# Optimization experiments

Hardware: AMD Instinct MI355X
Metric: run time of the kernel (lower is better)

## Reference

```python
import jax, jax.numpy as jnp
import numpy as np

N_NODES = 100000
N_EDGES = 1600000
IN_C, HID_C, OUT_C = 256, 128, 40
NEG_SLOPE = 0.2


def _gat_conv(x, W, att_l, att_r, b, src, dst, n_nodes):
    # x: [N, in], W: [out, in] (torch Linear layout)
    xl = x @ W.T                                  # [N, C]
    alpha_l = (xl * att_l).sum(-1)                # [N]
    alpha_r = (xl * att_r).sum(-1)                # [N]
    e = alpha_l[src] + alpha_r[dst]               # [E]
    e = jax.nn.leaky_relu(e, NEG_SLOPE)
    # segment softmax over destination nodes
    seg_max = jax.ops.segment_max(e, dst, num_segments=n_nodes)
    seg_max = jnp.where(jnp.isfinite(seg_max), seg_max, 0.0)
    ex = jnp.exp(e - seg_max[dst])
    denom = jax.ops.segment_sum(ex, dst, num_segments=n_nodes)
    alpha = ex / jnp.maximum(denom, 1e-16)[dst]   # [E]
    msgs = xl[src] * alpha[:, None]               # [E, C]
    out = jax.ops.segment_sum(msgs, dst, num_segments=n_nodes)
    return out + b


def setup_inputs() -> dict:
    key = jax.random.key(0)
    ks = jax.random.split(key, 9)
    def glorot(k, shape, fan):
        return jax.random.normal(k, shape, jnp.float32) * (1.0 / np.sqrt(fan))
    x = jax.random.normal(ks[0], (N_NODES, IN_C), jnp.float32)
    edge_index = jax.random.randint(ks[1], (2, N_EDGES), 0, N_NODES, jnp.int32)
    return {
        "x": x,
        "edge_index": edge_index,
        "W1": glorot(ks[2], (HID_C, IN_C), IN_C),
        "att_l1": glorot(ks[3], (HID_C,), HID_C),
        "att_r1": glorot(ks[4], (HID_C,), HID_C),
        "b1": jnp.zeros((HID_C,), jnp.float32),
        "W2": glorot(ks[5], (OUT_C, HID_C), HID_C),
        "att_l2": glorot(ks[6], (OUT_C,), OUT_C),
        "att_r2": glorot(ks[7], (OUT_C,), OUT_C),
        "b2": jnp.zeros((OUT_C,), jnp.float32),
    }


def reference(x, edge_index, W1, att_l1, att_r1, b1, W2, att_l2, att_r2, b2):
    src, dst = edge_index[0], edge_index[1]
    n = x.shape[0]
    # eval mode: dropout is identity
    h = _gat_conv(x, W1, att_l1, att_r1, b1, src, dst, n)
    h = jax.nn.elu(h)
    h = _gat_conv(h, W2, att_l2, att_r2, b2, src, dst, n)
    return jax.nn.log_softmax(h, axis=1)
```

## Files before the change

kernel.cpp:

```cpp
#include <hip/hip_runtime.h>
#include <hip/hip_bf16.h>

#define N_NODES 100000
#define N_EDGES 1600000
#define IN_C 256
#define HID_C 128
#define OUT_C 40
#define NB1 391

typedef short bf16x8 __attribute__((ext_vector_type(8)));
typedef float f32x4 __attribute__((ext_vector_type(4)));

__device__ __forceinline__ float lrelu(float x) { return x > 0.f ? x : 0.2f * x; }
__device__ __forceinline__ float eluf(float x) { return x > 0.f ? x : expm1f(x); }
__device__ __forceinline__ unsigned short f2bf(float f) {
    unsigned u = __float_as_uint(f);
    unsigned r = (u + 0x7FFFu + ((u >> 16) & 1u)) >> 16;
    return (unsigned short)r;
}

__global__ __launch_bounds__(256) void zero_cnt_kernel(unsigned* __restrict__ cnt)
{
    int i = blockIdx.x * 256 + threadIdx.x;
    if (i < N_NODES) cnt[i] = 0u;
}

__global__ __launch_bounds__(256) void rank_kernel(const int* __restrict__ dst,
                                                   unsigned* __restrict__ cnt,
                                                   unsigned* __restrict__ rank)
{
    int e4 = (blockIdx.x * 256 + threadIdx.x) * 4;
    if (e4 >= N_EDGES) return;
    int4 d = *(const int4*)(dst + e4);
    uint4 r;
    r.x = atomicAdd(&cnt[d.x], 1u);
    r.y = atomicAdd(&cnt[d.y], 1u);
    r.z = atomicAdd(&cnt[d.z], 1u);
    r.w = atomicAdd(&cnt[d.w], 1u);
    *(uint4*)(rank + e4) = r;
}

__global__ __launch_bounds__(256) void scan1_kernel(const unsigned* __restrict__ cnt,
                                                    unsigned* __restrict__ partial,
                                                    unsigned* __restrict__ blocksum)
{
    int gid = blockIdx.x * 256 + threadIdx.x;
    unsigned v = (gid < N_NODES) ? cnt[gid] : 0u;
    unsigned orig = v;
    int lane = threadIdx.x & 63, w = threadIdx.x >> 6;
#pragma unroll
    for (int o = 1; o < 64; o <<= 1) {
        unsigned t = __shfl_up(v, o);
        if (lane >= o) v += t;
    }
    __shared__ unsigned wsum[4];
    if (lane == 63) wsum[w] = v;
    __syncthreads();
    unsigned off = 0;
    for (int i = 0; i < w; ++i) off += wsum[i];
    v += off;
    if (gid < N_NODES) partial[gid] = v - orig;
    if (threadIdx.x == 255) blocksum[blockIdx.x] = v;
}

__global__ __launch_bounds__(512) void scan2_kernel(unsigned* __restrict__ blocksum)
{
    int tid = threadIdx.x;
    unsigned v = (tid < NB1) ? blocksum[tid] : 0u;
    unsigned orig = v;
    int lane = tid & 63, w = tid >> 6;
#pragma unroll
    for (int o = 1; o < 64; o <<= 1) {
        unsigned t = __shfl_up(v, o);
        if (lane >= o) v += t;
    }
    __shared__ unsigned wsum[8];
    if (lane == 63) wsum[w] = v;
    __syncthreads();
    unsigned off = 0;
    for (int i = 0; i < w; ++i) off += wsum[i];
    v += off;
    if (tid < NB1) blocksum[tid] = v - orig;
}

__global__ __launch_bounds__(256) void scan3_kernel(const unsigned* __restrict__ partial,
                                                    const unsigned* __restrict__ blocksum,
                                                    unsigned* __restrict__ row_start)
{
    int gid = blockIdx.x * 256 + threadIdx.x;
    if (gid < N_NODES) row_start[gid] = partial[gid] + blocksum[gid >> 8];
}

__global__ __launch_bounds__(256) void place_kernel(const int* __restrict__ src,
                                                    const int* __restrict__ dst,
                                                    const unsigned* __restrict__ rank,
                                                    const unsigned* __restrict__ row_start,
                                                    int* __restrict__ csr_src)
{
    int e4 = (blockIdx.x * 256 + threadIdx.x) * 4;
    if (e4 >= N_EDGES) return;
    int4 d = *(const int4*)(dst + e4);
    int4 s = *(const int4*)(src + e4);
    uint4 r = *(const uint4*)(rank + e4);
    csr_src[row_start[d.x] + r.x] = s.x;
    csr_src[row_start[d.y] + r.y] = s.y;
    csr_src[row_start[d.z] + r.z] = s.z;
    csr_src[row_start[d.w] + r.w] = s.w;
}

template <int KD, int PC>
__global__ __launch_bounds__(256) void prep_w_kernel(const float* __restrict__ W,
                                                     unsigned short* __restrict__ Wb,
                                                     int realC)
{
    int idx = blockIdx.x * 256 + threadIdx.x;
    if (idx >= PC * KD) return;
    int ch = idx / KD;
    int k = idx & (KD - 1);
    float v = (ch < realC) ? W[(size_t)ch * KD + k] : 0.f;
    Wb[idx] = f2bf(v);
}

template <int KD, int NT, int COLS>
__global__ __launch_bounds__(256) void gemm_mfma_kernel(
    const float* __restrict__ A, const unsigned short* __restrict__ Wb,
    float* __restrict__ out)
{
    int tid = threadIdx.x;
    int wv = tid >> 6, lane = tid & 63;
    int bm = blockIdx.x * 64 + wv * 16;
    int r = lane & 15;
    int kg = lane >> 4;

    f32x4 acc[NT];
#pragma unroll
    for (int n = 0; n < NT; ++n) acc[n] = (f32x4){0.f, 0.f, 0.f, 0.f};

    int arow = bm + r; if (arow >= N_NODES) arow = N_NODES - 1;
    const float* ap = A + (size_t)arow * KD + kg * 8;
    const unsigned short* bp = Wb + (size_t)r * KD + kg * 8;

    for (int ks = 0; ks < KD / 32; ++ks) {
        float4 a0 = *(const float4*)(ap);
        float4 a1 = *(const float4*)(ap + 4);
        bf16x8 af;
        af[0] = (short)f2bf(a0.x); af[1] = (short)f2bf(a0.y);
        af[2] = (short)f2bf(a0.z); af[3] = (short)f2bf(a0.w);
        af[4] = (short)f2bf(a1.x); af[5] = (short)f2bf(a1.y);
        af[6] = (short)f2bf(a1.z); af[7] = (short)f2bf(a1.w);
#pragma unroll
        for (int n = 0; n < NT; ++n) {
            bf16x8 bf_ = *(const bf16x8*)(bp + (size_t)n * 16 * KD);
            acc[n] = __builtin_amdgcn_mfma_f32_16x16x32_bf16(af, bf_, acc[n], 0, 0, 0);
        }
        ap += 32; bp += 32;
    }

#pragma unroll
    for (int n = 0; n < NT; ++n) {
        int col = n * 16 + r;
        if (col < COLS) {
#pragma unroll
            for (int rr = 0; rr < 4; ++rr) {
                int node = bm + kg * 4 + rr;
                if (node < N_NODES) out[(size_t)node * COLS + col] = acc[n][rr];
            }
        }
    }
}

template <int C>
__global__ __launch_bounds__(256) void alphas_kernel(
    const float* __restrict__ xl, const float* __restrict__ attl,
    const float* __restrict__ attr, float* __restrict__ al, float* __restrict__ ar)
{
    int wid = blockIdx.x * 4 + (threadIdx.x >> 6);
    int lane = threadIdx.x & 63;
    if (wid >= N_NODES) return;
    const float* row = xl + (size_t)wid * C;
    float sl = 0.f, sr = 0.f;
    if (lane < C) { float v = row[lane]; sl += v * attl[lane]; sr += v * attr[lane]; }
    if (C > 64 && lane + 64 < C) { float v = row[lane + 64]; sl += v * attl[lane + 64]; sr += v * attr[lane + 64]; }
#pragma unroll
    for (int o = 32; o > 0; o >>= 1) { sl += __shfl_xor(sl, o); sr += __shfl_xor(sr, o); }
    if (lane == 0) { al[wid] = sl; ar[wid] = sr; }
}

template <int C, int MODE>
__global__ __launch_bounds__(256) void agg_kernel(
    const int* __restrict__ csr_src,
    const unsigned* __restrict__ row_start, const unsigned* __restrict__ deg,
    const float* __restrict__ al, const float* __restrict__ ar,
    const float* __restrict__ xl, const float* __restrict__ bias,
    float* __restrict__ outp)
{
    int node = blockIdx.x * 4 + (threadIdx.x >> 6);
    int lane = threadIdx.x & 63;
    if (node >= N_NODES) return;
    unsigned beg = row_start[node];
    unsigned end = beg + deg[node];
    float ar_d = ar[node];

    unsigned i0 = beg + lane;
    float e0 = (i0 < end) ? lrelu(al[csr_src[i0]] + ar_d) : -INFINITY;
    float m_l = e0;
    for (unsigned i = i0 + 64; i < end; i += 64)
        m_l = fmaxf(m_l, lrelu(al[csr_src[i]] + ar_d));
    float mx = m_l;
#pragma unroll
    for (int o = 32; o > 0; o >>= 1) mx = fmaxf(mx, __shfl_xor(mx, o));
    float s_l = (i0 < end) ? __expf(e0 - mx) : 0.f;
    for (unsigned i = i0 + 64; i < end; i += 64)
        s_l += __expf(lrelu(al[csr_src[i]] + ar_d) - mx);
    float sm = s_l;
#pragma unroll
    for (int o = 32; o > 0; o >>= 1) sm += __shfl_xor(sm, o);
    float inv = 1.f / fmaxf(sm, 1e-16f);

    float acc0 = 0.f, acc1 = 0.f;
    unsigned i = beg;
    for (; i + 4 <= end; i += 4) {
        int s0 = csr_src[i], s1 = csr_src[i + 1], s2 = csr_src[i + 2], s3 = csr_src[i + 3];
        float w0 = __expf(lrelu(al[s0] + ar_d) - mx);
        float w1 = __expf(lrelu(al[s1] + ar_d) - mx);
        float w2 = __expf(lrelu(al[s2] + ar_d) - mx);
        float w3 = __expf(lrelu(al[s3] + ar_d) - mx);
        const float* p0 = xl + (size_t)s0 * C;
        const float* p1 = xl + (size_t)s1 * C;
        const float* p2 = xl + (size_t)s2 * C;
        const float* p3 = xl + (size_t)s3 * C;
        if (C > 64) {
            acc0 += p0[lane] * w0;      acc1 += p0[lane + 64] * w0;
            acc0 += p1[lane] * w1;      acc1 += p1[lane + 64] * w1;
            acc0 += p2[lane] * w2;      acc1 += p2[lane + 64] * w2;
            acc0 += p3[lane] * w3;      acc1 += p3[lane + 64] * w3;
        } else if (lane < C) {
            acc0 += p0[lane] * w0 + p1[lane] * w1 + p2[lane] * w2 + p3[lane] * w3;
        }
    }
    for (; i < end; ++i) {
        int s0 = csr_src[i];
        float w0 = __expf(lrelu(al[s0] + ar_d) - mx);
        const float* p0 = xl + (size_t)s0 * C;
        if (C > 64) { acc0 += p0[lane] * w0; acc1 += p0[lane + 64] * w0; }
        else if (lane < C) acc0 += p0[lane] * w0;
    }
    acc0 *= inv; acc1 *= inv;

    if (MODE == 0) {
        outp[(size_t)node * C + lane]      = eluf(acc0 + bias[lane]);
        outp[(size_t)node * C + lane + 64] = eluf(acc1 + bias[lane + 64]);
    } else {
        float v = (lane < C) ? (acc0 + bias[lane]) : -INFINITY;
        float m = v;
#pragma unroll
        for (int o = 32; o > 0; o >>= 1) m = fmaxf(m, __shfl_xor(m, o));
        float ex = (lane < C) ? __expf(v - m) : 0.f;
        float ssum = ex;
#pragma unroll
        for (int o = 32; o > 0; o >>= 1) ssum += __shfl_xor(ssum, o);
        if (lane < C) outp[(size_t)node * C + lane] = v - m - logf(ssum);
    }
}

extern "C" void kernel_launch(void* const* d_in, const int* in_sizes, int n_in,
                              void* d_out, int out_size, void* d_ws, size_t ws_size,
                              hipStream_t stream)
{
    const float* x    = (const float*)d_in[0];
    const int*   ei   = (const int*)d_in[1];
    const float* W1   = (const float*)d_in[2];
    const float* atl1 = (const float*)d_in[3];
    const float* atr1 = (const float*)d_in[4];
    const float* b1   = (const float*)d_in[5];
    const float* W2   = (const float*)d_in[6];
    const float* atl2 = (const float*)d_in[7];
    const float* atr2 = (const float*)d_in[8];
    const float* b2   = (const float*)d_in[9];
    float* out = (float*)d_out;
    const int* src = ei;
    const int* dst = ei + N_EDGES;
    (void)ws_size; (void)n_in; (void)in_sizes; (void)out_size;

    float* ws = (float*)d_ws;
    float* xl1      = ws;
    float* h        = xl1 + (size_t)N_NODES * HID_C;
    float* xl2      = h   + (size_t)N_NODES * HID_C;
    float* al1      = xl2 + (size_t)N_NODES * OUT_C;
    float* ar1      = al1 + N_NODES;
    float* al2      = ar1 + N_NODES;
    float* ar2      = al2 + N_NODES;
    unsigned* cnt      = (unsigned*)(ar2 + N_NODES);
    unsigned* partial  = cnt + N_NODES;
    unsigned* blocksum = partial + N_NODES;
    unsigned* row_start= blocksum + 512;
    int*      csr_src  = (int*)(row_start + N_NODES);
    unsigned short* W1b = (unsigned short*)(csr_src + N_EDGES);
    unsigned short* W2b = W1b + HID_C * IN_C;
    unsigned* rank = (unsigned*)xl2;

    const int EB4 = (N_EDGES / 4 + 255) / 256;
    const int NB4 = (N_NODES + 3) / 4;

    zero_cnt_kernel<<<NB1, 256, 0, stream>>>(cnt);
    rank_kernel<<<EB4, 256, 0, stream>>>(dst, cnt, rank);
    scan1_kernel<<<NB1, 256, 0, stream>>>(cnt, partial, blocksum);
    scan2_kernel<<<1, 512, 0, stream>>>(blocksum);
    scan3_kernel<<<NB1, 256, 0, stream>>>(partial, blocksum, row_start);
    place_kernel<<<EB4, 256, 0, stream>>>(src, dst, rank, row_start, csr_src);

    prep_w_kernel<IN_C, HID_C><<<(HID_C * IN_C + 255) / 256, 256, 0, stream>>>(W1, W1b, HID_C);
    prep_w_kernel<HID_C, 48><<<(48 * HID_C + 255) / 256, 256, 0, stream>>>(W2, W2b, OUT_C);

    gemm_mfma_kernel<IN_C, 8, HID_C><<<(N_NODES + 63) / 64, 256, 0, stream>>>(x, W1b, xl1);
    alphas_kernel<HID_C><<<NB4, 256, 0, stream>>>(xl1, atl1, atr1, al1, ar1);
    agg_kernel<HID_C, 0><<<NB4, 256, 0, stream>>>(
        csr_src, row_start, cnt, al1, ar1, xl1, b1, h);

    gemm_mfma_kernel<HID_C, 3, OUT_C><<<(N_NODES + 63) / 64, 256, 0, stream>>>(h, W2b, xl2);
    alphas_kernel<OUT_C><<<NB4, 256, 0, stream>>>(xl2, atl2, atr2, al2, ar2);
    agg_kernel<OUT_C, 1><<<NB4, 256, 0, stream>>>(
        csr_src, row_start, cnt, al2, ar2, xl2, b2, out);
}
```

Baseline: 599.4 us.

## Store intermediate node features in bf16 to halve gather traffic

The projected features xl1, the hidden activations h and xl2 are now stored as bf16 instead of fp32. The aggregation and alpha kernels read packed bf16 pairs per lane. The second GEMM consumes bf16 directly, which removes the in-loop conversion. The goal is to cut memory bandwidth in the edge-gather aggregation, the dominant cost, at the price of lower precision in the intermediates.

```diff
diff --git a/kernel.cpp b/kernel.cpp
--- a/kernel.cpp
+++ b/kernel.cpp
@@ -18,6 +18,8 @@
     unsigned r = (u + 0x7FFFu + ((u >> 16) & 1u)) >> 16;
     return (unsigned short)r;
 }
+__device__ __forceinline__ float bf_lo(unsigned u) { return __uint_as_float(u << 16); }
+__device__ __forceinline__ float bf_hi(unsigned u) { return __uint_as_float(u & 0xFFFF0000u); }
 
 __global__ __launch_bounds__(256) void zero_cnt_kernel(unsigned* __restrict__ cnt)
 {
@@ -121,11 +123,11 @@
     Wb[idx] = f2bf(v);
 }
 
-template <int KD, int NT, int COLS>
-__global__ __launch_bounds__(256) void gemm_mfma_kernel(
+__global__ __launch_bounds__(256) void gemm1_mfma_kernel(
     const float* __restrict__ A, const unsigned short* __restrict__ Wb,
-    float* __restrict__ out)
-{
+    unsigned short* __restrict__ outb)
+{
+    const int KD = IN_C, NT = 8, COLS = HID_C;
     int tid = threadIdx.x;
     int wv = tid >> 6, lane = tid & 63;
     int bm = blockIdx.x * 64 + wv * 16;
@@ -159,11 +161,51 @@
 #pragma unroll
     for (int n = 0; n < NT; ++n) {
         int col = n * 16 + r;
+#pragma unroll
+        for (int rr = 0; rr < 4; ++rr) {
+            int node = bm + kg * 4 + rr;
+            if (node < N_NODES) outb[(size_t)node * COLS + col] = f2bf(acc[n][rr]);
+        }
+    }
+}
+
+__global__ __launch_bounds__(256) void gemm2_mfma_kernel(
+    const unsigned short* __restrict__ Ab, const unsigned short* __restrict__ Wb,
+    unsigned short* __restrict__ outb)
+{
+    const int KD = HID_C, NT = 3, COLS = OUT_C;
+    int tid = threadIdx.x;
+    int wv = tid >> 6, lane = tid & 63;
+    int bm = blockIdx.x * 64 + wv * 16;
+    int r = lane & 15;
+    int kg = lane >> 4;
+
+    f32x4 acc[NT];
+#pragma unroll
+    for (int n = 0; n < NT; ++n) acc[n] = (f32x4){0.f, 0.f, 0.f, 0.f};
+
+    int arow = bm + r; if (arow >= N_NODES) arow = N_NODES - 1;
+    const unsigned short* ap = Ab + (size_t)arow * KD + kg * 8;
+    const unsigned short* bp = Wb + (size_t)r * KD + kg * 8;
+
+    for (int ks = 0; ks < KD / 32; ++ks) {
+        bf16x8 af = *(const bf16x8*)(ap);
+#pragma unroll
+        for (int n = 0; n < NT; ++n) {
+            bf16x8 bf_ = *(const bf16x8*)(bp + (size_t)n * 16 * KD);
+            acc[n] = __builtin_amdgcn_mfma_f32_16x16x32_bf16(af, bf_, acc[n], 0, 0, 0);
+        }
+        ap += 32; bp += 32;
+    }
+
+#pragma unroll
+    for (int n = 0; n < NT; ++n) {
+        int col = n * 16 + r;
         if (col < COLS) {
 #pragma unroll
             for (int rr = 0; rr < 4; ++rr) {
                 int node = bm + kg * 4 + rr;
-                if (node < N_NODES) out[(size_t)node * COLS + col] = acc[n][rr];
+                if (node < N_NODES) outb[(size_t)node * COLS + col] = f2bf(acc[n][rr]);
             }
         }
     }
@@ -171,16 +213,19 @@
 
 template <int C>
 __global__ __launch_bounds__(256) void alphas_kernel(
-    const float* __restrict__ xl, const float* __restrict__ attl,
+    const unsigned short* __restrict__ xlb, const float* __restrict__ attl,
     const float* __restrict__ attr, float* __restrict__ al, float* __restrict__ ar)
 {
     int wid = blockIdx.x * 4 + (threadIdx.x >> 6);
     int lane = threadIdx.x & 63;
     if (wid >= N_NODES) return;
-    const float* row = xl + (size_t)wid * C;
     float sl = 0.f, sr = 0.f;
-    if (lane < C) { float v = row[lane]; sl += v * attl[lane]; sr += v * attr[lane]; }
-    if (C > 64 && lane + 64 < C) { float v = row[lane + 64]; sl += v * attl[lane + 64]; sr += v * attr[lane + 64]; }
+    if (2 * lane < C) {
+        unsigned u = *(const unsigned*)(xlb + (size_t)wid * C + 2 * lane);
+        float lo = bf_lo(u), hi = bf_hi(u);
+        sl += lo * attl[2 * lane] + hi * attl[2 * lane + 1];
+        sr += lo * attr[2 * lane] + hi * attr[2 * lane + 1];
+    }
 #pragma unroll
     for (int o = 32; o > 0; o >>= 1) { sl += __shfl_xor(sl, o); sr += __shfl_xor(sr, o); }
     if (lane == 0) { al[wid] = sl; ar[wid] = sr; }
@@ -191,8 +236,8 @@
     const int* __restrict__ csr_src,
     const unsigned* __restrict__ row_start, const unsigned* __restrict__ deg,
     const float* __restrict__ al, const float* __restrict__ ar,
-    const float* __restrict__ xl, const float* __restrict__ bias,
-    float* __restrict__ outp)
+    const unsigned short* __restrict__ xlb, const float* __restrict__ bias,
+    void* __restrict__ outp)
 {
     int node = blockIdx.x * 4 + (threadIdx.x >> 6);
     int lane = threadIdx.x & 63;
@@ -217,7 +262,8 @@
     for (int o = 32; o > 0; o >>= 1) sm += __shfl_xor(sm, o);
     float inv = 1.f / fmaxf(sm, 1e-16f);
 
-    float acc0 = 0.f, acc1 = 0.f;
+    const bool act = (2 * lane < C);
+    float acc_lo = 0.f, acc_hi = 0.f;
     unsigned i = beg;
     for (; i + 4 <= end; i += 4) {
         int s0 = csr_src[i], s1 = csr_src[i + 1], s2 = csr_src[i + 2], s3 = csr_src[i + 3];
@@ -225,41 +271,46 @@
         float w1 = __expf(lrelu(al[s1] + ar_d) - mx);
         float w2 = __expf(lrelu(al[s2] + ar_d) - mx);
         float w3 = __expf(lrelu(al[s3] + ar_d) - mx);
-        const float* p0 = xl + (size_t)s0 * C;
-        const float* p1 = xl + (size_t)s1 * C;
-        const float* p2 = xl + (size_t)s2 * C;
-        const float* p3 = xl + (size_t)s3 * C;
-        if (C > 64) {
-            acc0 += p0[lane] * w0;      acc1 += p0[lane + 64] * w0;
-            acc0 += p1[lane] * w1;      acc1 += p1[lane + 64] * w1;
-            acc0 += p2[lane] * w2;      acc1 += p2[lane + 64] * w2;
-            acc0 += p3[lane] * w3;      acc1 += p3[lane + 64] * w3;
-        } else if (lane < C) {
-            acc0 += p0[lane] * w0 + p1[lane] * w1 + p2[lane] * w2 + p3[lane] * w3;
+        if (act) {
+            unsigned u0 = *(const unsigned*)(xlb + (size_t)s0 * C + 2 * lane);
+            unsigned u1 = *(const unsigned*)(xlb + (size_t)s1 * C + 2 * lane);
+            unsigned u2 = *(const unsigned*)(xlb + (size_t)s2 * C + 2 * lane);
+            unsigned u3 = *(const unsigned*)(xlb + (size_t)s3 * C + 2 * lane);
+            acc_lo += bf_lo(u0) * w0 + bf_lo(u1) * w1 + bf_lo(u2) * w2 + bf_lo(u3) * w3;
+            acc_hi += bf_hi(u0) * w0 + bf_hi(u1) * w1 + bf_hi(u2) * w2 + bf_hi(u3) * w3;
         }
     }
     for (; i < end; ++i) {
         int s0 = csr_src[i];
         float w0 = __expf(lrelu(al[s0] + ar_d) - mx);
-        const float* p0 = xl + (size_t)s0 * C;
-        if (C > 64) { acc0 += p0[lane] * w0; acc1 += p0[lane + 64] * w0; }
-        else if (lane < C) acc0 += p0[lane] * w0;
-    }
-    acc0 *= inv; acc1 *= inv;
+        if (act) {
+            unsigned u0 = *(const unsigned*)(xlb + (size_t)s0 * C + 2 * lane);
+            acc_lo += bf_lo(u0) * w0;
+            acc_hi += bf_hi(u0) * w0;
+        }
+    }
+    acc_lo *= inv; acc_hi *= inv;
 
     if (MODE == 0) {
-        outp[(size_t)node * C + lane]      = eluf(acc0 + bias[lane]);
-        outp[(size_t)node * C + lane + 64] = eluf(acc1 + bias[lane + 64]);
+        float vlo = eluf(acc_lo + bias[2 * lane]);
+        float vhi = eluf(acc_hi + bias[2 * lane + 1]);
+        unsigned p = ((unsigned)f2bf(vhi) << 16) | (unsigned)f2bf(vlo);
+        *(unsigned*)((unsigned short*)outp + (size_t)node * C + 2 * lane) = p;
     } else {
-        float v = (lane < C) ? (acc0 + bias[lane]) : -INFINITY;
-        float m = v;
+        float vlo = act ? (acc_lo + bias[2 * lane])     : -INFINITY;
+        float vhi = act ? (acc_hi + bias[2 * lane + 1]) : -INFINITY;
+        float m = fmaxf(vlo, vhi);
 #pragma unroll
         for (int o = 32; o > 0; o >>= 1) m = fmaxf(m, __shfl_xor(m, o));
-        float ex = (lane < C) ? __expf(v - m) : 0.f;
+        float ex = act ? (__expf(vlo - m) + __expf(vhi - m)) : 0.f;
         float ssum = ex;
 #pragma unroll
         for (int o = 32; o > 0; o >>= 1) ssum += __shfl_xor(ssum, o);
-        if (lane < C) outp[(size_t)node * C + lane] = v - m - logf(ssum);
+        float lg = logf(ssum);
+        if (act) {
+            float2 o2 = make_float2(vlo - m - lg, vhi - m - lg);
+            *(float2*)((float*)outp + (size_t)node * C + 2 * lane) = o2;
+        }
     }
 }
 
@@ -282,22 +333,22 @@
     const int* dst = ei + N_EDGES;
     (void)ws_size; (void)n_in; (void)in_sizes; (void)out_size;
 
-    float* ws = (float*)d_ws;
-    float* xl1      = ws;
-    float* h        = xl1 + (size_t)N_NODES * HID_C;
-    float* xl2      = h   + (size_t)N_NODES * HID_C;
-    float* al1      = xl2 + (size_t)N_NODES * OUT_C;
-    float* ar1      = al1 + N_NODES;
-    float* al2      = ar1 + N_NODES;
-    float* ar2      = al2 + N_NODES;
-    unsigned* cnt      = (unsigned*)(ar2 + N_NODES);
-    unsigned* partial  = cnt + N_NODES;
-    unsigned* blocksum = partial + N_NODES;
-    unsigned* row_start= blocksum + 512;
-    int*      csr_src  = (int*)(row_start + N_NODES);
+    char* wsb = (char*)d_ws;
+    unsigned short* xlb  = (unsigned short*)wsb;
+    unsigned short* hb   = xlb + (size_t)N_NODES * HID_C;
+    unsigned short* xl2b = hb  + (size_t)N_NODES * HID_C;
+    float* al1 = (float*)(xl2b + (size_t)N_NODES * OUT_C);
+    float* ar1 = al1 + N_NODES;
+    float* al2 = ar1 + N_NODES;
+    float* ar2 = al2 + N_NODES;
+    unsigned* cnt       = (unsigned*)(ar2 + N_NODES);
+    unsigned* partial   = cnt + N_NODES;
+    unsigned* blocksum  = partial + N_NODES;
+    unsigned* row_start = blocksum + 512;
+    int*      csr_src   = (int*)(row_start + N_NODES);
     unsigned short* W1b = (unsigned short*)(csr_src + N_EDGES);
     unsigned short* W2b = W1b + HID_C * IN_C;
-    unsigned* rank = (unsigned*)xl2;
+    unsigned* rank = (unsigned*)hb;
 
     const int EB4 = (N_EDGES / 4 + 255) / 256;
     const int NB4 = (N_NODES + 3) / 4;
@@ -312,13 +363,13 @@
     prep_w_kernel<IN_C, HID_C><<<(HID_C * IN_C + 255) / 256, 256, 0, stream>>>(W1, W1b, HID_C);
     prep_w_kernel<HID_C, 48><<<(48 * HID_C + 255) / 256, 256, 0, stream>>>(W2, W2b, OUT_C);
 
-    gemm_mfma_kernel<IN_C, 8, HID_C><<<(N_NODES + 63) / 64, 256, 0, stream>>>(x, W1b, xl1);
-    alphas_kernel<HID_C><<<NB4, 256, 0, stream>>>(xl1, atl1, atr1, al1, ar1);
+    gemm1_mfma_kernel<<<(N_NODES + 63) / 64, 256, 0, stream>>>(x, W1b, xlb);
+    alphas_kernel<HID_C><<<NB4, 256, 0, stream>>>(xlb, atl1, atr1, al1, ar1);
     agg_kernel<HID_C, 0><<<NB4, 256, 0, stream>>>(
-        csr_src, row_start, cnt, al1, ar1, xl1, b1, h);
-
-    gemm_mfma_kernel<HID_C, 3, OUT_C><<<(N_NODES + 63) / 64, 256, 0, stream>>>(h, W2b, xl2);
-    alphas_kernel<OUT_C><<<NB4, 256, 0, stream>>>(xl2, atl2, atr2, al2, ar2);
+        csr_src, row_start, cnt, al1, ar1, xlb, b1, hb);
+
+    gemm2_mfma_kernel<<<(N_NODES + 63) / 64, 256, 0, stream>>>(hb, W2b, xl2b);
+    alphas_kernel<OUT_C><<<NB4, 256, 0, stream>>>(xl2b, atl2, atr2, al2, ar2);
     agg_kernel<OUT_C, 1><<<NB4, 256, 0, stream>>>(
-        csr_src, row_start, cnt, al2, ar2, xl2, b2, out);
-}
+        csr_src, row_start, cnt, al2, ar2, xl2b, b2, out);
+}
```

Measured after the change: 576.8 us. 3.8% less time.
